# Optimization experiments

Measured on AMD Instinct MI355X. Metric: run time of the kernel, lower is better.

## Reference

```python
import jax, jax.numpy as jnp
import numpy as np

EPS = 1e-5  # torch BatchNorm default eps
SLOPE = 0.2  # LeakyReLU negative slope


def bn_apply(h, p):
    # p: (4, C) stacked [gamma, beta, running_mean, running_var]; h channel-last
    g, b, m, v = p[0], p[1], p[2], p[3]
    return (h - m) * (g * jax.lax.rsqrt(v + EPS)) + b


def graph_feature(x, k):
    # x: (B, N, C) -> (B, N, k, 2C) = concat(neighbor - center, center)
    inner = jnp.einsum('bnc,bmc->bnm', x, x)
    sq = jnp.sum(x * x, axis=-1)
    # negative squared pairwise distance (B, N, N)
    pd = 2.0 * inner - sq[:, :, None] - sq[:, None, :]
    idx = jax.lax.top_k(pd, k)[1]  # (B, N, k)
    nbr = jax.vmap(lambda xb, ib: xb[ib])(x, idx)  # (B, N, k, C) gather
    ctr = jnp.broadcast_to(x[:, :, None, :], nbr.shape)
    return jnp.concatenate([nbr - ctr, ctr], axis=-1)


def edge_block(h, w, bnp, k):
    # h: (B, N, C); w: (O, 2C) 1x1 conv weight; returns (B, N, O) after max over k
    f = graph_feature(h, k)
    z = jnp.einsum('bnkc,oc->bnko', f, w)
    z = jax.nn.leaky_relu(bn_apply(z, bnp), SLOPE)
    return jnp.max(z, axis=2)


def setup_inputs() -> dict:
    key = jax.random.key(0)
    ks = jax.random.split(key, 10)
    B, N, K = 16, 1024, 20
    emb, ncls = 1024, 40

    def bnp(c):
        return jnp.stack([jnp.ones(c), jnp.zeros(c), jnp.zeros(c), jnp.ones(c)])

    s = 0.05
    return {
        'x': jax.random.normal(ks[0], (B, 3, N), dtype=jnp.float32),
        'w1': jax.random.normal(ks[1], (64, 6), dtype=jnp.float32) * s,
        'bn1': bnp(64),
        'w2': jax.random.normal(ks[2], (64, 128), dtype=jnp.float32) * s,
        'bn2': bnp(64),
        'w3': jax.random.normal(ks[3], (128, 128), dtype=jnp.float32) * s,
        'bn3': bnp(128),
        'w4': jax.random.normal(ks[4], (256, 256), dtype=jnp.float32) * s,
        'bn4': bnp(256),
        'w5': jax.random.normal(ks[5], (emb, 512), dtype=jnp.float32) * s,
        'bn5': bnp(emb),
        'wl1': jax.random.normal(ks[6], (512, 2 * emb), dtype=jnp.float32) * s,
        'bn6': bnp(512),
        'wl2': jax.random.normal(ks[7], (256, 512), dtype=jnp.float32) * s,
        'bn7': bnp(256),
        'wl3': jax.random.normal(ks[8], (ncls, 256), dtype=jnp.float32) * s,
        'bl3': jax.random.normal(ks[9], (ncls,), dtype=jnp.float32) * s,
        'k': K,
    }


def reference(x, w1, bn1, w2, bn2, w3, bn3, w4, bn4, w5, bn5,
              wl1, bn6, wl2, bn7, wl3, bl3, k):
    # x: (B, 3, N) -> logits (B, num_classes); eval-mode BN, dropout = identity
    h0 = jnp.transpose(x, (0, 2, 1))  # (B, N, 3)
    x1 = edge_block(h0, w1, bn1, k)   # (B, N, 64)
    x2 = edge_block(x1, w2, bn2, k)   # (B, N, 64)
    x3 = edge_block(x2, w3, bn3, k)   # (B, N, 128)
    x4 = edge_block(x3, w4, bn4, k)   # (B, N, 256)
    h = jnp.concatenate([x1, x2, x3, x4], axis=-1)  # (B, N, 512)
    h = jax.nn.leaky_relu(bn_apply(jnp.einsum('bnc,oc->bno', h, w5), bn5), SLOPE)
    p = jnp.concatenate([jnp.max(h, axis=1), jnp.mean(h, axis=1)], axis=-1)  # (B, 2*emb)
    h = jax.nn.leaky_relu(bn_apply(p @ wl1.T, bn6), SLOPE)
    h = jax.nn.leaky_relu(bn_apply(h @ wl2.T, bn7), SLOPE)
    return h @ wl3.T + bl3
```

## Files before the change

### kernel.cpp

```cpp
#include <hip/hip_runtime.h>

#define BB 16
#define NN 1024
#define KNN 20
#define BNEPS 1e-5f

typedef __attribute__((ext_vector_type(8))) short short8;
typedef __attribute__((ext_vector_type(4))) float f32x4;

__device__ __forceinline__ float4 ld4(const float* p){ return *(const float4*)p; }
__device__ __forceinline__ void fma4(float4& a, float s, float4 w){
  a.x = fmaf(s, w.x, a.x); a.y = fmaf(s, w.y, a.y);
  a.z = fmaf(s, w.z, a.z); a.w = fmaf(s, w.w, a.w);
}
__device__ __forceinline__ void max4(float4& a, float4 v){
  a.x = fmaxf(a.x, v.x); a.y = fmaxf(a.y, v.y);
  a.z = fmaxf(a.z, v.z); a.w = fmaxf(a.w, v.w);
}
__device__ __forceinline__ unsigned short f2bf(float f){
  unsigned int u = __float_as_uint(f);
  u = (u + 0x7FFF + ((u >> 16) & 1)) >> 16;
  return (unsigned short)u;
}
__device__ __forceinline__ f32x4 mfma16(short8 a, short8 b, f32x4 c){
  return __builtin_amdgcn_mfma_f32_16x16x32_bf16(a, b, c, 0, 0, 0);
}

__device__ __forceinline__ void top3_build(const float* rp, int kmr,
                                           float& a0, float& a1, float& a2,
                                           int& i0, int& i1, int& i2){
  a0 = -1e30f; a1 = -1e30f; a2 = -1e30f; i0 = 0; i1 = 0; i2 = 0;
#pragma unroll
  for (int r = 0; r < 4; r++){
    float4 t = ld4(rp + r*4);
    float tv[4] = {t.x, t.y, t.z, t.w};
#pragma unroll
    for (int q = 0; q < 4; q++){
      int e = r*4 + q;
      float v = ((kmr >> e) & 1) ? -1e30f : tv[q];
      bool b0 = v > a0, b1 = v > a1, b2 = v > a2;
      a2 = b1 ? a1 : (b2 ? v : a2); i2 = b1 ? i1 : (b2 ? e : i2);
      a1 = b0 ? a0 : (b1 ? v : a1); i1 = b0 ? i0 : (b1 ? e : i1);
      a0 = b0 ? v  : a0;            i0 = b0 ? e : i0;
    }
  }
}

__global__ __launch_bounds__(256) void k_transpose(const float* __restrict__ x, float* __restrict__ xt,
                                                   float* __restrict__ sq){
  int i = blockIdx.x*256 + threadIdx.x;
  if (i >= BB*NN) return;
  int b = i >> 10, n = i & 1023;
  const float* xb = x + (size_t)b*3*NN;
  float4 v;
  v.x = xb[0*NN+n]; v.y = xb[1*NN+n]; v.z = xb[2*NN+n]; v.w = 0.f;
  ((float4*)xt)[i] = v;
  sq[i] = v.x*v.x + v.y*v.y + v.z*v.z;
}

__device__ __forceinline__ void prep_w_dev(int i, const float* w, const float* bnp,
                                           float* wlT, float* dT, float* bias, int Cin, int Cpad, int Cout){
  if (i >= Cpad*Cout) return;
  int c = i / Cout, o = i - c*Cout;
  float s = bnp[o] * rsqrtf(bnp[3*Cout+o] + BNEPS);
  float wl = (c < Cin) ? w[(size_t)o*2*Cin + c] : 0.f;
  float wr = (c < Cin) ? w[(size_t)o*2*Cin + Cin + c] : 0.f;
  wlT[i] = wl * s;
  dT[i]  = (wr - wl) * s;
  if (c == 0) bias[o] = bnp[Cout+o] - bnp[2*Cout+o]*s;
}
__device__ __forceinline__ void prep_wbf_dev(int i, const float* w, const float* bnp,
                                             unsigned short* wlB, unsigned short* dB, float* bias,
                                             int Cin, int Cout){
  if (i >= Cin*Cout) return;
  int o = i / Cin, c = i - o*Cin;
  float s = bnp[o] * rsqrtf(bnp[3*Cout+o] + BNEPS);
  float wl = w[(size_t)o*2*Cin + c] * s;
  float wr = w[(size_t)o*2*Cin + Cin + c] * s;
  wlB[i] = f2bf(wl);
  dB[i]  = f2bf(wr - wl);
  if (c == 0) bias[o] = bnp[Cout+o] - bnp[2*Cout+o]*s;
}

__global__ __launch_bounds__(256) void k_prep_all(const float* __restrict__ w1, const float* __restrict__ bn1,
                                                  const float* __restrict__ w2, const float* __restrict__ bn2,
                                                  const float* __restrict__ w3, const float* __restrict__ bn3,
                                                  const float* __restrict__ w4, const float* __restrict__ bn4,
                                                  const float* __restrict__ w5, const float* __restrict__ bn5,
                                                  float* __restrict__ wlT1, float* __restrict__ dT1, float* __restrict__ bias1,
                                                  unsigned short* __restrict__ wlB2, unsigned short* __restrict__ dB2, float* __restrict__ bias2,
                                                  unsigned short* __restrict__ wlB3, unsigned short* __restrict__ dB3, float* __restrict__ bias3,
                                                  unsigned short* __restrict__ wlB4, unsigned short* __restrict__ dB4, float* __restrict__ bias4,
                                                  unsigned short* __restrict__ w5b, float* __restrict__ b5){
  int bid = blockIdx.x, t = threadIdx.x;
  if (bid < 1){
    prep_w_dev(t, w1, bn1, wlT1, dT1, bias1, 3, 4, 64);
  } else if (bid < 17){
    prep_wbf_dev((bid-1)*256 + t, w2, bn2, wlB2, dB2, bias2, 64, 64);
  } else if (bid < 49){
    prep_wbf_dev((bid-17)*256 + t, w3, bn3, wlB3, dB3, bias3, 64, 128);
  } else if (bid < 177){
    prep_wbf_dev((bid-49)*256 + t, w4, bn4, wlB4, dB4, bias4, 128, 256);
  } else {
    int i = (bid-177)*256 + t;
    int o = i >> 9, c = i & 511;
    float s = bn5[o] * rsqrtf(bn5[3*1024+o] + BNEPS);
    w5b[i] = f2bf(w5[(size_t)o*512 + c] * s);
    if (c == 0) b5[o] = bn5[1024+o] - bn5[2*1024+o]*s;
  }
}

__global__ __launch_bounds__(256) void k_sq(const float* __restrict__ xin, int rs, int Cin, float* __restrict__ sq){
  int i = blockIdx.x*256 + threadIdx.x;
  if (i >= BB*NN) return;
  const float* r = xin + (size_t)i*rs;
  float s = 0.f;
  for (int c = 0; c < Cin; c += 4){
    float4 v = ld4(r + c);
    s += v.x*v.x + v.y*v.y + v.z*v.z + v.w*v.w;
  }
  sq[i] = s;
}

__global__ __launch_bounds__(256) void k_pd(const float* __restrict__ xin, int rs, int Cin, int CT, int lnf4,
                                            const float* __restrict__ sq, float* __restrict__ pd){
  extern __shared__ float lds[];
  const int pitch = CT + 4;
  float* As = lds;
  float* Bs = lds + 64*pitch;
  const int b = blockIdx.y;
  int t = blockIdx.x, ti = 0;
  while (t >= 16 - ti){ t -= (16 - ti); ti++; }
  const int tj = ti + t;
  const int n0 = ti*64, m0 = tj*64;
  const int tid = threadIdx.x;
  const int tx = tid & 15, ty = tid >> 4;
  const float* xb = xin + (size_t)b*NN*rs;
  float acc[4][4];
#pragma unroll
  for (int i = 0; i < 4; i++)
#pragma unroll
    for (int j = 0; j < 4; j++) acc[i][j] = 0.f;

  const int nf4 = CT >> 2;
  for (int c0 = 0; c0 < Cin; c0 += CT){
    for (int e = tid; e < 64*nf4; e += 256){
      int r = e >> lnf4, cc = (e & (nf4-1))*4;
      *(float4*)(As + r*pitch + cc) = ld4(xb + (size_t)(n0+r)*rs + c0 + cc);
      *(float4*)(Bs + r*pitch + cc) = ld4(xb + (size_t)(m0+r)*rs + c0 + cc);
    }
    __syncthreads();
    for (int c = 0; c < CT; c += 4){
      float4 a[4], bv[4];
#pragma unroll
      for (int i = 0; i < 4; i++) a[i]  = ld4(As + (ty+16*i)*pitch + c);
#pragma unroll
      for (int j = 0; j < 4; j++) bv[j] = ld4(Bs + (tx+16*j)*pitch + c);
#pragma unroll
      for (int i = 0; i < 4; i++)
#pragma unroll
        for (int j = 0; j < 4; j++){
          acc[i][j] = fmaf(a[i].x, bv[j].x, acc[i][j]);
          acc[i][j] = fmaf(a[i].y, bv[j].y, acc[i][j]);
          acc[i][j] = fmaf(a[i].z, bv[j].z, acc[i][j]);
          acc[i][j] = fmaf(a[i].w, bv[j].w, acc[i][j]);
        }
    }
    __syncthreads();
  }

#pragma unroll
  for (int i = 0; i < 4; i++){
    int n = n0 + ty + 16*i;
#pragma unroll
    for (int j = 0; j < 4; j++){
      int m = m0 + tx + 16*j;
      pd[((size_t)b*NN + n)*NN + m] = 2.f*acc[i][j] - sq[b*NN + m];
    }
  }

  if (ti != tj){
    const int PT = 68;
    float* Ltr = lds;
    float sqn[4];
#pragma unroll
    for (int i = 0; i < 4; i++) sqn[i] = sq[b*NN + n0 + ty + 16*i];
#pragma unroll
    for (int i = 0; i < 4; i++)
#pragma unroll
      for (int j = 0; j < 4; j++)
        Ltr[(tx + 16*j)*PT + ty + 16*i] = 2.f*acc[i][j] - sqn[i];
    __syncthreads();
    for (int e = tid; e < 64*16; e += 256){
      int r = e >> 4, c4 = (e & 15)*4;
      *(float4*)(pd + ((size_t)b*NN + m0 + r)*NN + n0 + c4) = *(float4*)(Ltr + r*PT + c4);
    }
  }
}

__global__ __launch_bounds__(256) void k_topk(const float* __restrict__ pd, int* __restrict__ idxOut){
  int w = threadIdx.x >> 6, lane = threadIdx.x & 63;
  int bn0 = (blockIdx.x*4 + w)*2;
  const float* row0 = pd + (size_t)bn0*NN + lane*16;
  const float* row1 = row0 + NN;

  float c0v[2], c1v[2], c2v[2];
  int   c0i[2], c1i[2], c2i[2];
  int   km[2] = {0, 0};
  top3_build(row0, 0, c0v[0], c1v[0], c2v[0], c0i[0], c1i[0], c2i[0]);
  top3_build(row1, 0, c0v[1], c1v[1], c2v[1], c0i[1], c1i[1], c2i[1]);

  int* out0 = idxOut + (size_t)bn0*KNN;
  int* out1 = out0 + KNN;
  for (int it = 0; it < KNN; it++){
    float g0 = c0v[0], g1 = c0v[1];
#pragma unroll
    for (int s = 1; s < 64; s <<= 1){
      g0 = fmaxf(g0, __shfl_xor(g0, s));
      g1 = fmaxf(g1, __shfl_xor(g1, s));
    }
    int o0 = __ffsll(__ballot(c0v[0] == g0)) - 1;
    int o1 = __ffsll(__ballot(c0v[1] == g1)) - 1;
    bool u0 = (lane == o0), u1 = (lane == o1);
    if (u0) out0[it] = lane*16 + c0i[0];
    if (u1) out1[it] = lane*16 + c0i[1];
    km[0] |= u0 ? (1 << c0i[0]) : 0;
    km[1] |= u1 ? (1 << c0i[1]) : 0;
    c0v[0] = u0 ? c1v[0] : c0v[0];  c0i[0] = u0 ? c1i[0] : c0i[0];
    c1v[0] = u0 ? c2v[0] : c1v[0];  c1i[0] = u0 ? c2i[0] : c1i[0];
    c2v[0] = u0 ? -1e30f : c2v[0];
    c0v[1] = u1 ? c1v[1] : c0v[1];  c0i[1] = u1 ? c1i[1] : c0i[1];
    c1v[1] = u1 ? c2v[1] : c1v[1];  c1i[1] = u1 ? c2i[1] : c1i[1];
    c2v[1] = u1 ? -1e30f : c2v[1];
    if (it < KNN-1){
      bool rp0 = (c0v[0] == -1e30f) && (km[0] != 0xFFFF);
      bool rp1 = (c0v[1] == -1e30f) && (km[1] != 0xFFFF);
      if (__ballot(rp0 || rp1)){
        if (rp0) top3_build(row0, km[0], c0v[0], c1v[0], c2v[0], c0i[0], c1i[0], c2i[0]);
        if (rp1) top3_build(row1, km[1], c0v[1], c1v[1], c2v[1], c0i[1], c1i[1], c2i[1]);
      }
    }
  }
}

__global__ __launch_bounds__(256) void k_uv1(const float* __restrict__ xt,
                                             const float* __restrict__ wlT, const float* __restrict__ dT,
                                             float* __restrict__ Z){
  int t = blockIdx.x*256 + threadIdx.x;
  int n = t >> 5, q = t & 31;
  float4 xv = ld4(xt + (size_t)n*4);
  const float* wp = (q < 16) ? (wlT + q*4) : (dT + (q-16)*4);
  float4 a = make_float4(0.f,0.f,0.f,0.f);
  fma4(a, xv.x, ld4(wp + 0*64));
  fma4(a, xv.y, ld4(wp + 1*64));
  fma4(a, xv.z, ld4(wp + 2*64));
  fma4(a, xv.w, ld4(wp + 3*64));
  *(float4*)(Z + (size_t)n*128 + q*4) = a;
}

template<int K>
__global__ __launch_bounds__(256) void k_uv(const unsigned short* __restrict__ hbi,
                                            const unsigned short* __restrict__ wB,
                                            float* __restrict__ Z, int ldz){
  __shared__ char sm[20480];
  char* As = sm; char* Bs = sm + 10240;
  const int tid = threadIdx.x, lane = tid & 63, w = tid >> 6;
  const int l15 = lane & 15, quad = lane >> 4;
  const int n0 = blockIdx.x*128, r0 = blockIdx.y*128;

  f32x4 acc[2][8];
  f32x4 zero = {0.f,0.f,0.f,0.f};
#pragma unroll
  for (int i = 0; i < 2; i++)
#pragma unroll
    for (int j = 0; j < 8; j++) acc[i][j] = zero;

  for (int k0 = 0; k0 < K; k0 += 32){
#pragma unroll
    for (int i = 0; i < 2; i++){
      int e = tid + i*256;
      int r = e >> 2, sg = e & 3;
      *(float4*)(As + r*80 + sg*16) = *(const float4*)(hbi + ((size_t)(r0+r))*512 + k0 + sg*8);
      *(float4*)(Bs + r*80 + sg*16) = *(const float4*)(wB  + ((size_t)(n0+r))*K   + k0 + sg*8);
    }
    __syncthreads();
    short8 af0 = *(short8*)(As + (w*32 + l15)*80 + quad*16);
    short8 af1 = *(short8*)(As + (w*32 + 16 + l15)*80 + quad*16);
#pragma unroll
    for (int ns = 0; ns < 8; ns++){
      short8 bf = *(short8*)(Bs + (ns*16 + l15)*80 + quad*16);
      acc[0][ns] = mfma16(af0, bf, acc[0][ns]);
      acc[1][ns] = mfma16(af1, bf, acc[1][ns]);
    }
    __syncthreads();
  }

#pragma unroll
  for (int ms = 0; ms < 2; ms++){
#pragma unroll
    for (int ns = 0; ns < 8; ns++){
      f32x4 a = acc[ms][ns];
      int row = r0 + w*32 + ms*16 + quad*4;
      int col = n0 + ns*16 + l15;
#pragma unroll
      for (int r = 0; r < 4; r++)
        Z[(size_t)(row+r)*ldz + col] = a[r];
    }
  }
}

template<int COUT, int P, bool WF32>
__global__ __launch_bounds__(256) void k_gmax(const float* __restrict__ Z,
                                              const float* __restrict__ bias,
                                              const int* __restrict__ knn_idx,
                                              float* __restrict__ hf,
                                              unsigned short* __restrict__ hbo){
  constexpr int QPP = COUT/4;
  __shared__ int idxS[P*KNN];
  const int tid = threadIdx.x;
  const int p0 = blockIdx.x * P;
  for (int t = tid; t < P*KNN; t += 256) idxS[t] = knn_idx[(size_t)p0*KNN + t];
  __syncthreads();

  const int p = tid / QPP, q = tid - p*QPP;
  const int base = p0 & ~1023;
  const int ldz = 2*COUT;
  const float* Zq = Z + q*4;

  float4 m = make_float4(-1e30f,-1e30f,-1e30f,-1e30f);
#pragma unroll
  for (int j = 0; j < KNN; j++){
    int mr = idxS[p*KNN + j];
    max4(m, ld4(Zq + (size_t)(base + mr)*ldz));
  }
  float4 ctr = ld4(Z + (size_t)(p0+p)*ldz + COUT + q*4);
  float4 bs  = ld4(bias + q*4);
  float4 y;
  y.x = m.x + ctr.x + bs.x; y.x = fmaxf(y.x, 0.2f*y.x);
  y.y = m.y + ctr.y + bs.y; y.y = fmaxf(y.y, 0.2f*y.y);
  y.z = m.z + ctr.z + bs.z; y.z = fmaxf(y.z, 0.2f*y.z);
  y.w = m.w + ctr.w + bs.w; y.w = fmaxf(y.w, 0.2f*y.w);

  size_t pi = (size_t)(p0 + p);
  if (WF32) *(float4*)(hf + pi*256 + q*4) = y;
  ushort4 hv; hv.x = f2bf(y.x); hv.y = f2bf(y.y); hv.z = f2bf(y.z); hv.w = f2bf(y.w);
  *(ushort4*)(hbo + pi*512 + q*4) = hv;
}

__global__ __launch_bounds__(256) void k_conv5m(const unsigned short* __restrict__ hb,
                                                const unsigned short* __restrict__ w5b,
                                                const float* __restrict__ b5,
                                                float* __restrict__ pmax, float* __restrict__ psum){
  __shared__ char sm[20480 + 4096];
  char* As = sm; char* Bs = sm + 10240;
  float* red = (float*)(sm + 20480);
  const int tid = threadIdx.x, lane = tid & 63, w = tid >> 6;
  const int l15 = lane & 15, quad = lane >> 4;
  const int n0 = blockIdx.x*128, r0 = blockIdx.y*128;

  f32x4 acc[2][8];
  f32x4 zero = {0.f,0.f,0.f,0.f};
#pragma unroll
  for (int i = 0; i < 2; i++)
#pragma unroll
    for (int j = 0; j < 8; j++) acc[i][j] = zero;

  for (int k0 = 0; k0 < 512; k0 += 32){
#pragma unroll
    for (int i = 0; i < 2; i++){
      int e = tid + i*256;
      int r = e >> 2, sg = e & 3;
      *(float4*)(As + r*80 + sg*16) = *(const float4*)(hb  + ((size_t)(r0+r))*512 + k0 + sg*8);
      *(float4*)(Bs + r*80 + sg*16) = *(const float4*)(w5b + ((size_t)(n0+r))*512 + k0 + sg*8);
    }
    __syncthreads();
    short8 af0 = *(short8*)(As + (w*32 + l15)*80 + quad*16);
    short8 af1 = *(short8*)(As + (w*32 + 16 + l15)*80 + quad*16);
#pragma unroll
    for (int ns = 0; ns < 8; ns++){
      short8 bf = *(short8*)(Bs + (ns*16 + l15)*80 + quad*16);
      acc[0][ns] = mfma16(af0, bf, acc[0][ns]);
      acc[1][ns] = mfma16(af1, bf, acc[1][ns]);
    }
    __syncthreads();
  }

#pragma unroll
  for (int ns = 0; ns < 8; ns++){
    float bv = b5[n0 + ns*16 + l15];
    float mx = -1e30f, sum = 0.f;
#pragma unroll
    for (int ms = 0; ms < 2; ms++){
      float* a = (float*)&acc[ms][ns];
#pragma unroll
      for (int r = 0; r < 4; r++){
        float v = a[r] + bv; v = fmaxf(v, 0.2f*v);
        mx = fmaxf(mx, v); sum += v;
      }
    }
    for (int s = 16; s < 64; s <<= 1){
      mx = fmaxf(mx, __shfl_xor(mx, s));
      sum += __shfl_xor(sum, s);
    }
    if (quad == 0){ red[(w*8 + ns)*16 + l15] = mx; red[512 + (w*8 + ns)*16 + l15] = sum; }
  }
  __syncthreads();
  if (tid < 128){
    int ns = tid >> 4, ci = tid & 15;
    float mx = -1e30f, sum = 0.f;
#pragma unroll
    for (int w2 = 0; w2 < 4; w2++){
      mx = fmaxf(mx, red[(w2*8 + ns)*16 + ci]);
      sum += red[512 + (w2*8 + ns)*16 + ci];
    }
    pmax[(size_t)blockIdx.y*1024 + n0 + tid] = mx;
    psum[(size_t)blockIdx.y*1024 + n0 + tid] = sum;
  }
}

__global__ __launch_bounds__(256) void k_fc1(const float* __restrict__ pmax, const float* __restrict__ psum,
                                             const float* __restrict__ wl1, const float* __restrict__ bn6,
                                             float* __restrict__ h1){
  __shared__ float pS[2048];
  const int b = blockIdx.y, t = threadIdx.x;
  for (int f = t; f < 512; f += 256){
    float4 r;
    if (f < 256){
      r = ld4(pmax + (size_t)(b*8)*1024 + f*4);
#pragma unroll
      for (int ch = 1; ch < 8; ch++) max4(r, ld4(pmax + (size_t)(b*8+ch)*1024 + f*4));
    } else {
      int o = (f-256)*4;
      r = ld4(psum + (size_t)(b*8)*1024 + o);
#pragma unroll
      for (int ch = 1; ch < 8; ch++){
        float4 s = ld4(psum + (size_t)(b*8+ch)*1024 + o);
        r.x += s.x; r.y += s.y; r.z += s.z; r.w += s.w;
      }
      r.x *= (1.f/1024.f); r.y *= (1.f/1024.f); r.z *= (1.f/1024.f); r.w *= (1.f/1024.f);
    }
    ((float4*)pS)[f] = r;
  }
  __syncthreads();
  const int ol = t >> 4, ch = t & 15;
  const int o = blockIdx.x*16 + ol;
  const float* wr = wl1 + (size_t)o*2048;
  float acc = 0.f;
#pragma unroll
  for (int j = 0; j < 32; j++){
    int c = ch*4 + j*64;
    float4 wv = ld4(wr + c);
    acc += pS[c]*wv.x + pS[c+1]*wv.y + pS[c+2]*wv.z + pS[c+3]*wv.w;
  }
#pragma unroll
  for (int s = 1; s < 16; s <<= 1) acc += __shfl_xor(acc, s);
  if (ch == 0){
    float s = bn6[o] * rsqrtf(bn6[3*512+o] + BNEPS);
    float y = (acc - bn6[2*512+o])*s + bn6[512+o];
    h1[(size_t)b*512 + o] = fmaxf(y, 0.2f*y);
  }
}

__global__ __launch_bounds__(256) void k_fc2(const float* __restrict__ h1,
                                             const float* __restrict__ wl2, const float* __restrict__ bn7,
                                             float* __restrict__ h2){
  __shared__ float hS[512];
  const int b = blockIdx.y, t = threadIdx.x;
  if (t < 128) ((float4*)hS)[t] = ((const float4*)(h1 + (size_t)b*512))[t];
  __syncthreads();
  const int ol = t >> 4, ch = t & 15;
  const int o = blockIdx.x*16 + ol;
  const float* wr = wl2 + (size_t)o*512;
  float acc = 0.f;
#pragma unroll
  for (int j = 0; j < 8; j++){
    int c = ch*4 + j*64;
    float4 wv = ld4(wr + c);
    acc += hS[c]*wv.x + hS[c+1]*wv.y + hS[c+2]*wv.z + hS[c+3]*wv.w;
  }
#pragma unroll
  for (int s = 1; s < 16; s <<= 1) acc += __shfl_xor(acc, s);
  if (ch == 0){
    float s = bn7[o] * rsqrtf(bn7[3*256+o] + BNEPS);
    float y = (acc - bn7[2*256+o])*s + bn7[256+o];
    h2[(size_t)b*256 + o] = fmaxf(y, 0.2f*y);
  }
}

__global__ __launch_bounds__(64) void k_fc3(const float* __restrict__ h2,
                                            const float* __restrict__ wl3, const float* __restrict__ bl3,
                                            float* __restrict__ out){
  const int o = blockIdx.x, b = blockIdx.y, lane = threadIdx.x;
  float4 wv = ld4(wl3 + (size_t)o*256 + lane*4);
  float4 hv = ld4(h2 + (size_t)b*256 + lane*4);
  float acc = hv.x*wv.x + hv.y*wv.y + hv.z*wv.z + hv.w*wv.w;
#pragma unroll
  for (int s = 1; s < 64; s <<= 1) acc += __shfl_xor(acc, s);
  if (lane == 0) out[(size_t)b*40 + o] = acc + bl3[o];
}

extern "C" void kernel_launch(void* const* d_in, const int* in_sizes, int n_in,
                              void* d_out, int out_size, void* d_ws, size_t ws_size,
                              hipStream_t stream) {
  (void)in_sizes; (void)n_in; (void)out_size; (void)ws_size;
  const float* x   = (const float*)d_in[0];
  const float* w1  = (const float*)d_in[1];
  const float* bn1 = (const float*)d_in[2];
  const float* w2  = (const float*)d_in[3];
  const float* bn2 = (const float*)d_in[4];
  const float* w3  = (const float*)d_in[5];
  const float* bn3 = (const float*)d_in[6];
  const float* w4  = (const float*)d_in[7];
  const float* bn4 = (const float*)d_in[8];
  const float* w5  = (const float*)d_in[9];
  const float* bn5 = (const float*)d_in[10];
  const float* wl1 = (const float*)d_in[11];
  const float* bn6 = (const float*)d_in[12];
  const float* wl2 = (const float*)d_in[13];
  const float* bn7 = (const float*)d_in[14];
  const float* wl3 = (const float*)d_in[15];
  const float* bl3 = (const float*)d_in[16];
  float* out = (float*)d_out;

  float* ws    = (float*)d_ws;
  float* xt    = ws;
  float* sqb   = xt + 65536;
  int*   idxb  = (int*)(sqb + 16384);
  float* pd    = (float*)(idxb + 327680);
  float* h     = pd + 16777216;
  float* wlT1  = h + 4194304;
  float* dT1   = wlT1 + 256;
  float* bias1 = dT1 + 256;
  float* bias2 = bias1 + 64;
  float* bias3 = bias2 + 64;
  float* bias4 = bias3 + 128;
  float* b5    = bias4 + 256;
  float* pmax  = b5 + 1024;
  float* psum  = pmax + 131072;
  float* pool  = psum + 131072;
  float* h1b   = pool + 32768;
  float* h2b   = h1b + 8192;
  unsigned short* hb   = (unsigned short*)(h2b + 4096);
  unsigned short* wlB2 = hb + (size_t)16384*512;
  unsigned short* dB2  = wlB2 + 4096;
  unsigned short* wlB3 = dB2 + 4096;
  unsigned short* dB3  = wlB3 + 8192;
  unsigned short* wlB4 = dB3 + 8192;
  unsigned short* dB4  = wlB4 + 32768;
  unsigned short* w5b  = dB4 + 32768;
  float* Z = pd;

  k_transpose<<<64, 256, 0, stream>>>(x, xt, sqb);
  k_prep_all<<<2225, 256, 0, stream>>>(w1, bn1, w2, bn2, w3, bn3, w4, bn4, w5, bn5,
                                       wlT1, dT1, bias1, wlB2, dB2, bias2,
                                       wlB3, dB3, bias3, wlB4, dB4, bias4, w5b, b5);

  const size_t PD_LDS64 = 34816;
  const size_t PD_LDS4  = 17408;

  k_pd<<<dim3(136,16), 256, PD_LDS4, stream>>>(xt, 4, 4, 4, 0, sqb, pd);
  k_topk<<<2048, 256, 0, stream>>>(pd, idxb);
  k_uv1<<<2048, 256, 0, stream>>>(xt, wlT1, dT1, Z);
  k_gmax<64,16,true><<<1024, 256, 0, stream>>>(Z, bias1, idxb, h, hb);

  k_sq<<<64, 256, 0, stream>>>(h, 256, 64, sqb);
  k_pd<<<dim3(136,16), 256, PD_LDS64, stream>>>(h, 256, 64, 64, 4, sqb, pd);
  k_topk<<<2048, 256, 0, stream>>>(pd, idxb);
  k_uv<64><<<dim3(1,128), 256, 0, stream>>>(hb, wlB2, Z, 128);
  k_gmax<64,16,true><<<1024, 256, 0, stream>>>(Z, bias2, idxb, h + 64, hb + 64);

  k_sq<<<64, 256, 0, stream>>>(h + 64, 256, 64, sqb);
  k_pd<<<dim3(136,16), 256, PD_LDS64, stream>>>(h + 64, 256, 64, 64, 4, sqb, pd);
  k_topk<<<2048, 256, 0, stream>>>(pd, idxb);
  k_uv<64><<<dim3(2,128), 256, 0, stream>>>(hb + 64, wlB3, Z, 256);
  k_gmax<128,8,true><<<2048, 256, 0, stream>>>(Z, bias3, idxb, h + 128, hb + 128);

  k_sq<<<64, 256, 0, stream>>>(h + 128, 256, 128, sqb);
  k_pd<<<dim3(136,16), 256, PD_LDS64, stream>>>(h + 128, 256, 128, 64, 4, sqb, pd);
  k_topk<<<2048, 256, 0, stream>>>(pd, idxb);
  k_uv<128><<<dim3(4,128), 256, 0, stream>>>(hb + 128, wlB4, Z, 512);
  k_gmax<256,4,false><<<4096, 256, 0, stream>>>(Z, bias4, idxb, nullptr, hb + 256);

  k_conv5m<<<dim3(8,128), 256, 0, stream>>>(hb, w5b, b5, pmax, psum);
  k_fc1<<<dim3(32,16), 256, 0, stream>>>(pmax, psum, wl1, bn6, h1b);
  k_fc2<<<dim3(16,16), 256, 0, stream>>>(h1b, wl2, bn7, h2b);
  k_fc3<<<dim3(40,16), 64, 0, stream>>>(h2b, wl3, bl3, out);
}
```

Measured before the change: 465.8 us.

## Fuse pairwise-distance GEMM with top-k selection, keeping distance rows in registers

```diff
diff --git a/kernel.cpp b/kernel.cpp
--- a/kernel.cpp
+++ b/kernel.cpp
@@ -26,23 +26,17 @@
   return __builtin_amdgcn_mfma_f32_16x16x32_bf16(a, b, c, 0, 0, 0);
 }
 
-__device__ __forceinline__ void top3_build(const float* rp, int kmr,
-                                           float& a0, float& a1, float& a2,
-                                           int& i0, int& i1, int& i2){
+__device__ __forceinline__ void top3_reg(const float* v, int kmr,
+                                         float& a0, float& a1, float& a2,
+                                         int& i0, int& i1, int& i2){
   a0 = -1e30f; a1 = -1e30f; a2 = -1e30f; i0 = 0; i1 = 0; i2 = 0;
 #pragma unroll
-  for (int r = 0; r < 4; r++){
-    float4 t = ld4(rp + r*4);
-    float tv[4] = {t.x, t.y, t.z, t.w};
-#pragma unroll
-    for (int q = 0; q < 4; q++){
-      int e = r*4 + q;
-      float v = ((kmr >> e) & 1) ? -1e30f : tv[q];
-      bool b0 = v > a0, b1 = v > a1, b2 = v > a2;
-      a2 = b1 ? a1 : (b2 ? v : a2); i2 = b1 ? i1 : (b2 ? e : i2);
-      a1 = b0 ? a0 : (b1 ? v : a1); i1 = b0 ? i0 : (b1 ? e : i1);
-      a0 = b0 ? v  : a0;            i0 = b0 ? e : i0;
-    }
+  for (int e = 0; e < 16; e++){
+    float x = ((kmr >> e) & 1) ? -1e30f : v[e];
+    bool b0 = x > a0, b1 = x > a1, b2 = x > a2;
+    a2 = b1 ? a1 : (b2 ? x : a2); i2 = b1 ? i1 : (b2 ? e : i2);
+    a1 = b0 ? a0 : (b1 ? x : a1); i1 = b0 ? i0 : (b1 ? e : i1);
+    a0 = b0 ? x  : a0;            i0 = b0 ? e : i0;
   }
 }
 
@@ -122,122 +116,123 @@
   sq[i] = s;
 }
 
-__global__ __launch_bounds__(256) void k_pd(const float* __restrict__ xin, int rs, int Cin, int CT, int lnf4,
-                                            const float* __restrict__ sq, float* __restrict__ pd){
-  extern __shared__ float lds[];
-  const int pitch = CT + 4;
-  float* As = lds;
-  float* Bs = lds + 64*pitch;
-  const int b = blockIdx.y;
-  int t = blockIdx.x, ti = 0;
-  while (t >= 16 - ti){ t -= (16 - ti); ti++; }
-  const int tj = ti + t;
-  const int n0 = ti*64, m0 = tj*64;
+template<int K>
+__global__ __launch_bounds__(256) void k_pdtopk(const float* __restrict__ xin, int rs,
+                                                const float* __restrict__ sq,
+                                                int* __restrict__ idxOut){
+  extern __shared__ float Bs[];
   const int tid = threadIdx.x;
-  const int tx = tid & 15, ty = tid >> 4;
-  const float* xb = xin + (size_t)b*NN*rs;
-  float acc[4][4];
-#pragma unroll
-  for (int i = 0; i < 4; i++)
-#pragma unroll
-    for (int j = 0; j < 4; j++) acc[i][j] = 0.f;
-
-  const int nf4 = CT >> 2;
-  for (int c0 = 0; c0 < Cin; c0 += CT){
-    for (int e = tid; e < 64*nf4; e += 256){
-      int r = e >> lnf4, cc = (e & (nf4-1))*4;
-      *(float4*)(As + r*pitch + cc) = ld4(xb + (size_t)(n0+r)*rs + c0 + cc);
-      *(float4*)(Bs + r*pitch + cc) = ld4(xb + (size_t)(m0+r)*rs + c0 + cc);
-    }
-    __syncthreads();
-    for (int c = 0; c < CT; c += 4){
-      float4 a[4], bv[4];
-#pragma unroll
-      for (int i = 0; i < 4; i++) a[i]  = ld4(As + (ty+16*i)*pitch + c);
-#pragma unroll
-      for (int j = 0; j < 4; j++) bv[j] = ld4(Bs + (tx+16*j)*pitch + c);
-#pragma unroll
-      for (int i = 0; i < 4; i++)
-#pragma unroll
-        for (int j = 0; j < 4; j++){
-          acc[i][j] = fmaf(a[i].x, bv[j].x, acc[i][j]);
-          acc[i][j] = fmaf(a[i].y, bv[j].y, acc[i][j]);
-          acc[i][j] = fmaf(a[i].z, bv[j].z, acc[i][j]);
-          acc[i][j] = fmaf(a[i].w, bv[j].w, acc[i][j]);
+  const int lane = tid & 63, w = tid >> 6;
+  const int bn0 = blockIdx.x * 16;
+  const int base = (bn0 >> 10) << 10;
+  const int qsw = (lane >> 1) & 3;
+
+  float acc[4][16];
+#pragma unroll
+  for (int r = 0; r < 4; r++)
+#pragma unroll
+    for (int e = 0; e < 16; e++) acc[r][e] = 0.f;
+
+  if (K == 4){
+    float4 A4[4];
+#pragma unroll
+    for (int r = 0; r < 4; r++) A4[r] = ld4(xin + (size_t)(bn0 + w*4 + r)*4);
+#pragma unroll
+    for (int e = 0; e < 16; e++){
+      float4 Bv = ld4(xin + (size_t)(base + e*64 + lane)*4);
+#pragma unroll
+      for (int r = 0; r < 4; r++){
+        acc[r][e] = fmaf(A4[r].x, Bv.x, acc[r][e]);
+        acc[r][e] = fmaf(A4[r].y, Bv.y, acc[r][e]);
+        acc[r][e] = fmaf(A4[r].z, Bv.z, acc[r][e]);
+        acc[r][e] = fmaf(A4[r].w, Bv.w, acc[r][e]);
+      }
+    }
+  } else {
+#pragma unroll 1
+    for (int c0 = 0; c0 < K; c0 += 16){
+#pragma unroll 1
+      for (int half = 0; half < 2; half++){
+        __syncthreads();
+#pragma unroll
+        for (int it = 0; it < 8; it++){
+          int i = tid + it*256;
+          int mrow = (i >> 2);
+          int q = i & 3;
+          float4 v = ld4(xin + (size_t)(base + half*512 + mrow)*rs + c0 + q*4);
+          int qs = q ^ ((mrow >> 1) & 3);
+          *(float4*)(Bs + mrow*16 + qs*4) = v;
         }
-    }
-    __syncthreads();
-  }
-
-#pragma unroll
-  for (int i = 0; i < 4; i++){
-    int n = n0 + ty + 16*i;
-#pragma unroll
-    for (int j = 0; j < 4; j++){
-      int m = m0 + tx + 16*j;
-      pd[((size_t)b*NN + n)*NN + m] = 2.f*acc[i][j] - sq[b*NN + m];
-    }
-  }
-
-  if (ti != tj){
-    const int PT = 68;
-    float* Ltr = lds;
-    float sqn[4];
-#pragma unroll
-    for (int i = 0; i < 4; i++) sqn[i] = sq[b*NN + n0 + ty + 16*i];
-#pragma unroll
-    for (int i = 0; i < 4; i++)
-#pragma unroll
-      for (int j = 0; j < 4; j++)
-        Ltr[(tx + 16*j)*PT + ty + 16*i] = 2.f*acc[i][j] - sqn[i];
-    __syncthreads();
-    for (int e = tid; e < 64*16; e += 256){
-      int r = e >> 4, c4 = (e & 15)*4;
-      *(float4*)(pd + ((size_t)b*NN + m0 + r)*NN + n0 + c4) = *(float4*)(Ltr + r*PT + c4);
-    }
-  }
-}
-
-__global__ __launch_bounds__(256) void k_topk(const float* __restrict__ pd, int* __restrict__ idxOut){
-  int w = threadIdx.x >> 6, lane = threadIdx.x & 63;
-  int bn0 = (blockIdx.x*4 + w)*2;
-  const float* row0 = pd + (size_t)bn0*NN + lane*16;
-  const float* row1 = row0 + NN;
-
-  float c0v[2], c1v[2], c2v[2];
-  int   c0i[2], c1i[2], c2i[2];
-  int   km[2] = {0, 0};
-  top3_build(row0, 0, c0v[0], c1v[0], c2v[0], c0i[0], c1i[0], c2i[0]);
-  top3_build(row1, 0, c0v[1], c1v[1], c2v[1], c0i[1], c1i[1], c2i[1]);
-
-  int* out0 = idxOut + (size_t)bn0*KNN;
-  int* out1 = out0 + KNN;
-  for (int it = 0; it < KNN; it++){
-    float g0 = c0v[0], g1 = c0v[1];
-#pragma unroll
-    for (int s = 1; s < 64; s <<= 1){
-      g0 = fmaxf(g0, __shfl_xor(g0, s));
-      g1 = fmaxf(g1, __shfl_xor(g1, s));
-    }
-    int o0 = __ffsll(__ballot(c0v[0] == g0)) - 1;
-    int o1 = __ffsll(__ballot(c0v[1] == g1)) - 1;
-    bool u0 = (lane == o0), u1 = (lane == o1);
-    if (u0) out0[it] = lane*16 + c0i[0];
-    if (u1) out1[it] = lane*16 + c0i[1];
-    km[0] |= u0 ? (1 << c0i[0]) : 0;
-    km[1] |= u1 ? (1 << c0i[1]) : 0;
-    c0v[0] = u0 ? c1v[0] : c0v[0];  c0i[0] = u0 ? c1i[0] : c0i[0];
-    c1v[0] = u0 ? c2v[0] : c1v[0];  c1i[0] = u0 ? c2i[0] : c1i[0];
-    c2v[0] = u0 ? -1e30f : c2v[0];
-    c0v[1] = u1 ? c1v[1] : c0v[1];  c0i[1] = u1 ? c1i[1] : c0i[1];
-    c1v[1] = u1 ? c2v[1] : c1v[1];  c1i[1] = u1 ? c2i[1] : c1i[1];
-    c2v[1] = u1 ? -1e30f : c2v[1];
-    if (it < KNN-1){
-      bool rp0 = (c0v[0] == -1e30f) && (km[0] != 0xFFFF);
-      bool rp1 = (c0v[1] == -1e30f) && (km[1] != 0xFFFF);
-      if (__ballot(rp0 || rp1)){
-        if (rp0) top3_build(row0, km[0], c0v[0], c1v[0], c2v[0], c0i[0], c1i[0], c2i[0]);
-        if (rp1) top3_build(row1, km[1], c0v[1], c1v[1], c2v[1], c0i[1], c1i[1], c2i[1]);
+        __syncthreads();
+#pragma unroll
+        for (int k4 = 0; k4 < 4; k4++){
+          float4 A4[4];
+#pragma unroll
+          for (int r = 0; r < 4; r++)
+            A4[r] = ld4(xin + (size_t)(bn0 + w*4 + r)*rs + c0 + k4*4);
+          int qs = k4 ^ qsw;
+#pragma unroll
+          for (int eg = 0; eg < 8; eg++){
+            float4 Bv = *(float4*)(Bs + (lane + 64*eg)*16 + qs*4);
+            int e = half*8 + eg;
+#pragma unroll
+            for (int r = 0; r < 4; r++){
+              acc[r][e] = fmaf(A4[r].x, Bv.x, acc[r][e]);
+              acc[r][e] = fmaf(A4[r].y, Bv.y, acc[r][e]);
+              acc[r][e] = fmaf(A4[r].z, Bv.z, acc[r][e]);
+              acc[r][e] = fmaf(A4[r].w, Bv.w, acc[r][e]);
+            }
+          }
+        }
+      }
+    }
+  }
+
+#pragma unroll
+  for (int e = 0; e < 16; e++){
+    float sqm = sq[base + e*64 + lane];
+#pragma unroll
+    for (int r = 0; r < 4; r++) acc[r][e] = 2.f*acc[r][e] - sqm;
+  }
+
+#pragma unroll
+  for (int pp = 0; pp < 2; pp++){
+    const float* v0 = acc[pp*2];
+    const float* v1 = acc[pp*2+1];
+    float c0v[2], c1v[2], c2v[2];
+    int   c0i[2], c1i[2], c2i[2];
+    int   km[2] = {0, 0};
+    top3_reg(v0, 0, c0v[0], c1v[0], c2v[0], c0i[0], c1i[0], c2i[0]);
+    top3_reg(v1, 0, c0v[1], c1v[1], c2v[1], c0i[1], c1i[1], c2i[1]);
+    int* out0 = idxOut + (size_t)(bn0 + w*4 + pp*2)*KNN;
+    int* out1 = out0 + KNN;
+    for (int it = 0; it < KNN; it++){
+      float g0 = c0v[0], g1 = c0v[1];
+#pragma unroll
+      for (int s = 1; s < 64; s <<= 1){
+        g0 = fmaxf(g0, __shfl_xor(g0, s));
+        g1 = fmaxf(g1, __shfl_xor(g1, s));
+      }
+      int o0 = __ffsll(__ballot(c0v[0] == g0)) - 1;
+      int o1 = __ffsll(__ballot(c0v[1] == g1)) - 1;
+      bool u0 = (lane == o0), u1 = (lane == o1);
+      if (u0) out0[it] = lane + (c0i[0] << 6);
+      if (u1) out1[it] = lane + (c0i[1] << 6);
+      km[0] |= u0 ? (1 << c0i[0]) : 0;
+      km[1] |= u1 ? (1 << c0i[1]) : 0;
+      c0v[0] = u0 ? c1v[0] : c0v[0];  c0i[0] = u0 ? c1i[0] : c0i[0];
+      c1v[0] = u0 ? c2v[0] : c1v[0];  c1i[0] = u0 ? c2i[0] : c1i[0];
+      c2v[0] = u0 ? -1e30f : c2v[0];
+      c0v[1] = u1 ? c1v[1] : c0v[1];  c0i[1] = u1 ? c1i[1] : c0i[1];
+      c1v[1] = u1 ? c2v[1] : c1v[1];  c1i[1] = u1 ? c2i[1] : c1i[1];
+      c2v[1] = u1 ? -1e30f : c2v[1];
+      if (it < KNN-1){
+        bool rp0 = (c0v[0] == -1e30f) && (km[0] != 0xFFFF);
+        bool rp1 = (c0v[1] == -1e30f) && (km[1] != 0xFFFF);
+        if (__ballot(rp0 || rp1)){
+          if (rp0) top3_reg(v0, km[0], c0v[0], c1v[0], c2v[0], c0i[0], c1i[0], c2i[0]);
+          if (rp1) top3_reg(v1, km[1], c0v[1], c1v[1], c2v[1], c0i[1], c1i[1], c2i[1]);
+        }
       }
     }
   }
@@ -263,7 +258,7 @@
                                             const unsigned short* __restrict__ wB,
                                             float* __restrict__ Z, int ldz){
   __shared__ char sm[20480];
-  char* As = sm; char* Bs = sm + 10240;
+  char* As = sm; char* Bsm = sm + 10240;
   const int tid = threadIdx.x, lane = tid & 63, w = tid >> 6;
   const int l15 = lane & 15, quad = lane >> 4;
   const int n0 = blockIdx.x*128, r0 = blockIdx.y*128;
@@ -281,14 +276,14 @@
       int e = tid + i*256;
       int r = e >> 2, sg = e & 3;
       *(float4*)(As + r*80 + sg*16) = *(const float4*)(hbi + ((size_t)(r0+r))*512 + k0 + sg*8);
-      *(float4*)(Bs + r*80 + sg*16) = *(const float4*)(wB  + ((size_t)(n0+r))*K   + k0 + sg*8);
+      *(float4*)(Bsm + r*80 + sg*16) = *(const float4*)(wB  + ((size_t)(n0+r))*K   + k0 + sg*8);
     }
     __syncthreads();
     short8 af0 = *(short8*)(As + (w*32 + l15)*80 + quad*16);
     short8 af1 = *(short8*)(As + (w*32 + 16 + l15)*80 + quad*16);
 #pragma unroll
     for (int ns = 0; ns < 8; ns++){
-      short8 bf = *(short8*)(Bs + (ns*16 + l15)*80 + quad*16);
+      short8 bf = *(short8*)(Bsm + (ns*16 + l15)*80 + quad*16);
       acc[0][ns] = mfma16(af0, bf, acc[0][ns]);
       acc[1][ns] = mfma16(af1, bf, acc[1][ns]);
     }
@@ -352,7 +347,7 @@
                                                 const float* __restrict__ b5,
                                                 float* __restrict__ pmax, float* __restrict__ psum){
   __shared__ char sm[20480 + 4096];
-  char* As = sm; char* Bs = sm + 10240;
+  char* As = sm; char* Bsm = sm + 10240;
   float* red = (float*)(sm + 20480);
   const int tid = threadIdx.x, lane = tid & 63, w = tid >> 6;
   const int l15 = lane & 15, quad = lane >> 4;
@@ -371,14 +366,14 @@
       int e = tid + i*256;
       int r = e >> 2, sg = e & 3;
       *(float4*)(As + r*80 + sg*16) = *(const float4*)(hb  + ((size_t)(r0+r))*512 + k0 + sg*8);
-      *(float4*)(Bs + r*80 + sg*16) = *(const float4*)(w5b + ((size_t)(n0+r))*512 + k0 + sg*8);
+      *(float4*)(Bsm + r*80 + sg*16) = *(const float4*)(w5b + ((size_t)(n0+r))*512 + k0 + sg*8);
     }
     __syncthreads();
     short8 af0 = *(short8*)(As + (w*32 + l15)*80 + quad*16);
     short8 af1 = *(short8*)(As + (w*32 + 16 + l15)*80 + quad*16);
 #pragma unroll
     for (int ns = 0; ns < 8; ns++){
-      short8 bf = *(short8*)(Bs + (ns*16 + l15)*80 + quad*16);
+      short8 bf = *(short8*)(Bsm + (ns*16 + l15)*80 + quad*16);
       acc[0][ns] = mfma16(af0, bf, acc[0][ns]);
       acc[1][ns] = mfma16(af1, bf, acc[1][ns]);
     }
@@ -555,29 +550,24 @@
                                        wlT1, dT1, bias1, wlB2, dB2, bias2,
                                        wlB3, dB3, bias3, wlB4, dB4, bias4, w5b, b5);
 
-  const size_t PD_LDS64 = 34816;
-  const size_t PD_LDS4  = 17408;
-
-  k_pd<<<dim3(136,16), 256, PD_LDS4, stream>>>(xt, 4, 4, 4, 0, sqb, pd);
-  k_topk<<<2048, 256, 0, stream>>>(pd, idxb);
+  const size_t PT_LDS = 512*16*4;
+
+  k_pdtopk<4><<<1024, 256, 0, stream>>>(xt, 4, sqb, idxb);
   k_uv1<<<2048, 256, 0, stream>>>(xt, wlT1, dT1, Z);
   k_gmax<64,16,true><<<1024, 256, 0, stream>>>(Z, bias1, idxb, h, hb);
 
   k_sq<<<64, 256, 0, stream>>>(h, 256, 64, sqb);
-  k_pd<<<dim3(136,16), 256, PD_LDS64, stream>>>(h, 256, 64, 64, 4, sqb, pd);
-  k_topk<<<2048, 256, 0, stream>>>(pd, idxb);
+  k_pdtopk<64><<<1024, 256, PT_LDS, stream>>>(h, 256, sqb, idxb);
   k_uv<64><<<dim3(1,128), 256, 0, stream>>>(hb, wlB2, Z, 128);
   k_gmax<64,16,true><<<1024, 256, 0, stream>>>(Z, bias2, idxb, h + 64, hb + 64);
 
   k_sq<<<64, 256, 0, stream>>>(h + 64, 256, 64, sqb);
-  k_pd<<<dim3(136,16), 256, PD_LDS64, stream>>>(h + 64, 256, 64, 64, 4, sqb, pd);
-  k_topk<<<2048, 256, 0, stream>>>(pd, idxb);
+  k_pdtopk<64><<<1024, 256, PT_LDS, stream>>>(h + 64, 256, sqb, idxb);
   k_uv<64><<<dim3(2,128), 256, 0, stream>>>(hb + 64, wlB3, Z, 256);
   k_gmax<128,8,true><<<2048, 256, 0, stream>>>(Z, bias3, idxb, h + 128, hb + 128);
 
   k_sq<<<64, 256, 0, stream>>>(h + 128, 256, 128, sqb);
-  k_pd<<<dim3(136,16), 256, PD_LDS64, stream>>>(h + 128, 256, 128, 64, 4, sqb, pd);
-  k_topk<<<2048, 256, 0, stream>>>(pd, idxb);
+  k_pdtopk<128><<<1024, 256, PT_LDS, stream>>>(h + 128, 256, sqb, idxb);
   k_uv<128><<<dim3(4,128), 256, 0, stream>>>(hb + 128, wlB4, Z, 512);
   k_gmax<256,4,false><<<4096, 256, 0, stream>>>(Z, bias4, idxb, nullptr, hb + 256);
 
```

Measured after the change: 1.398 ms. 3x slower.
